# Optimization experiments

Hardware: AMD Instinct MI355X
Metric: run time of the kernel (lower is better)

Reference implementation:

```python
import jax, jax.numpy as jnp
import numpy as np

EPS = 1e-6          # AllReduceParams.eps for the fused RMSNorm
FP8_MAX = 448.0     # max finite magnitude of float8_e4m3fn


def setup_inputs() -> dict:
    key = jax.random.key(0)
    k1, k2, k3 = jax.random.split(key, 3)
    tp, T, H = 4, 4096, 8192  # tp ranks, tokens, hidden
    return {
        "input": jax.random.normal(k1, (tp, T, H), jnp.float32) * 0.05,
        "residual": jax.random.normal(k2, (T, H), jnp.float32),
        "norm_weight": jax.random.uniform(k3, (H,), jnp.float32, 0.5, 1.5),
        "scale": jnp.ones((1,), jnp.float32),  # static per-tensor FP8 scale
    }


def _fp8_e4m3_roundtrip(x):
    # Emulate e4m3 rounding; straight-through so the op stays differentiable.
    x = jnp.clip(x, -FP8_MAX, FP8_MAX)
    rounded = x.astype(jnp.float8_e4m3fn).astype(jnp.float32)
    return x + jax.lax.stop_gradient(rounded - x)


def reference(input, residual, norm_weight, scale):
    # All-reduce (sum over TP ranks) -- leading axis models the TP group.
    reduced = jnp.sum(input, axis=0)                 # [T, H]
    # Fused residual add.
    residual_out = reduced + residual                # [T, H]
    # Fused RMSNorm.
    var = jnp.mean(jnp.square(residual_out), axis=-1, keepdims=True)
    norm = residual_out * jax.lax.rsqrt(var + EPS) * norm_weight
    # Fused static per-tensor FP8 (e4m3) quantization: q = round_fp8(x * scale).
    quant = _fp8_e4m3_roundtrip(norm * scale)        # [T, H] fp8-rounded values
    return (quant, residual_out)
```

## Files before the change

### kernel.cpp

```cpp
#include <hip/hip_runtime.h>

constexpr int TP  = 4;
constexpr int TT  = 4096;
constexpr int HH  = 8192;
constexpr int BLK = 512;
constexpr int NJ  = HH / (BLK * 4);

typedef float f32x4 __attribute__((ext_vector_type(4)));

__device__ __forceinline__ unsigned swz(unsigned byte) {
    return byte ^ (((byte >> 9) & 7u) << 4);
}

__device__ __forceinline__ double fp8_rne_d(double x) {
    long long b = (long long)__double_as_longlong(fabs(x));
    int ee = (int)(b >> 52);
    if (ee < 1017) ee = 1017;
    long long se = (long long)(ee - 3);
    double step = __longlong_as_double(se << 52);
    double inv  = __longlong_as_double((2046 - se) << 52);
    return rint(x * inv) * step;
}

__global__ __launch_bounds__(BLK) void fused_ar_rms_fp8(
    const float* __restrict__ input,
    const float* __restrict__ residual,
    const float* __restrict__ weight,
    const float* __restrict__ scale,
    float* __restrict__ quant,
    float* __restrict__ resid_out)
{
    __shared__ float lds[HH];
    __shared__ float bcast;

    const int t   = blockIdx.x;
    const int tid = threadIdx.x;
    const size_t row   = (size_t)t * HH;
    const size_t plane = (size_t)TT * HH;

    const f32x4* i0 = (const f32x4*)(input + row);
    const f32x4* i1 = (const f32x4*)(input + plane + row);
    const f32x4* i2 = (const f32x4*)(input + 2 * plane + row);
    const f32x4* i3 = (const f32x4*)(input + 3 * plane + row);
    const f32x4* rr = (const f32x4*)(residual + row);
    f32x4* qo = (f32x4*)(quant + row);
    f32x4* ro = (f32x4*)(resid_out + row);
    const f32x4* wv = (const f32x4*)weight;

    float s[NJ * 4];

    #pragma unroll
    for (int j = 0; j < NJ; ++j) {
        const int idx = j * BLK + tid;
        f32x4 a = i0[idx];
        f32x4 b = i1[idx];
        f32x4 c = i2[idx];
        f32x4 d = i3[idx];
        f32x4 r = rr[idx];
        f32x4 sv;
        #pragma unroll
        for (int k = 0; k < 4; ++k) {
            float v = __fadd_rn(a[k], b[k]);
            v = __fadd_rn(v, c[k]);
            v = __fadd_rn(v, d[k]);
            v = __fadd_rn(v, r[k]);
            sv[k] = v;
            s[j * 4 + k] = v;
        }
        const unsigned byte = 16u * (unsigned)idx;
        *(f32x4*)((char*)lds + swz(byte)) = sv;
        ro[idx] = sv;
    }
    __syncthreads();

    if (tid < 64) {
        const unsigned base = 512u * (unsigned)tid;
        float r8[8];
        f32x4 q0 = *(const f32x4*)((const char*)lds + swz(base));
        f32x4 q1 = *(const f32x4*)((const char*)lds + swz(base + 16));
        #pragma unroll
        for (int k = 0; k < 4; ++k) {
            r8[k]     = __fmul_rn(q0[k], q0[k]);
            r8[4 + k] = __fmul_rn(q1[k], q1[k]);
        }
        #pragma unroll
        for (int i = 1; i < 16; ++i) {
            const unsigned b2 = base + 32u * i;
            q0 = *(const f32x4*)((const char*)lds + swz(b2));
            q1 = *(const f32x4*)((const char*)lds + swz(b2 + 16));
            #pragma unroll
            for (int k = 0; k < 4; ++k) {
                r8[k]     = __fadd_rn(r8[k],     __fmul_rn(q0[k], q0[k]));
                r8[4 + k] = __fadd_rn(r8[4 + k], __fmul_rn(q1[k], q1[k]));
            }
        }
        float res = __fadd_rn(
            __fadd_rn(__fadd_rn(r8[0], r8[1]), __fadd_rn(r8[2], r8[3])),
            __fadd_rn(__fadd_rn(r8[4], r8[5]), __fadd_rn(r8[6], r8[7])));
        #pragma unroll
        for (int m = 1; m < 64; m <<= 1)
            res = __fadd_rn(res, __shfl_xor(res, m, 64));

        const float mean = __fmul_rn(res, 1.0f / 8192.0f);
        const float v    = __fadd_rn(mean, 1e-6f);
        const float rinv = __fdiv_rn(1.0f, __fsqrt_rn(v));
        if (tid == 0) bcast = rinv;
    }
    __syncthreads();

    const float rinv = bcast;
    const float sc   = scale[0];

    #pragma unroll
    for (int j = 0; j < NJ; ++j) {
        const int idx = j * BLK + tid;
        f32x4 w4 = wv[idx];
        f32x4 qv;
        #pragma unroll
        for (int k = 0; k < 4; ++k) {
            float n = __fmul_rn(s[j * 4 + k], rinv);
            n = __fmul_rn(n, w4[k]);
            n = __fmul_rn(n, sc);
            n = fminf(fmaxf(n, -448.0f), 448.0f);
            qv[k] = (float)fp8_rne_d((double)n);
        }
        qo[idx] = qv;
    }
}

extern "C" void kernel_launch(void* const* d_in, const int* in_sizes, int n_in,
                              void* d_out, int out_size, void* d_ws, size_t ws_size,
                              hipStream_t stream) {
    const float* input    = (const float*)d_in[0];
    const float* residual = (const float*)d_in[1];
    const float* weight   = (const float*)d_in[2];
    const float* scale    = (const float*)d_in[3];
    float* quant     = (float*)d_out;
    float* resid_out = (float*)d_out + (size_t)TT * HH;

    fused_ar_rms_fp8<<<TT, BLK, 0, stream>>>(input, residual, weight, scale,
                                             quant, resid_out);
}
```

Measured before the change: 178.4 us.

## Process four rows per block with register prefetch of next row and nontemporal IO

Result: slower. 209.8 us (+17.6%).

```diff
diff --git a/kernel.cpp b/kernel.cpp
--- a/kernel.cpp
+++ b/kernel.cpp
@@ -5,11 +5,19 @@
 constexpr int HH  = 8192;
 constexpr int BLK = 512;
 constexpr int NJ  = HH / (BLK * 4);
+constexpr int RPB = 4;
+constexpr int GRID = TT / RPB;
 
 typedef float f32x4 __attribute__((ext_vector_type(4)));
 
 __device__ __forceinline__ unsigned swz(unsigned byte) {
     return byte ^ (((byte >> 9) & 7u) << 4);
+}
+
+__device__ __forceinline__ void barrier_lgkm() {
+    asm volatile("s_waitcnt lgkmcnt(0)" ::: "memory");
+    __builtin_amdgcn_s_barrier();
+    asm volatile("" ::: "memory");
 }
 
 __device__ __forceinline__ double fp8_rne_d(double x) {
@@ -22,7 +30,7 @@
     return rint(x * inv) * step;
 }
 
-__global__ __launch_bounds__(BLK) void fused_ar_rms_fp8(
+__global__ __launch_bounds__(BLK, 4) void fused_ar_rms_fp8(
     const float* __restrict__ input,
     const float* __restrict__ residual,
     const float* __restrict__ weight,
@@ -33,98 +41,127 @@
     __shared__ float lds[HH];
     __shared__ float bcast;
 
-    const int t   = blockIdx.x;
     const int tid = threadIdx.x;
-    const size_t row   = (size_t)t * HH;
     const size_t plane = (size_t)TT * HH;
+    const size_t row0  = (size_t)blockIdx.x * RPB * HH;
 
-    const f32x4* i0 = (const f32x4*)(input + row);
-    const f32x4* i1 = (const f32x4*)(input + plane + row);
-    const f32x4* i2 = (const f32x4*)(input + 2 * plane + row);
-    const f32x4* i3 = (const f32x4*)(input + 3 * plane + row);
-    const f32x4* rr = (const f32x4*)(residual + row);
-    f32x4* qo = (f32x4*)(quant + row);
-    f32x4* ro = (f32x4*)(resid_out + row);
     const f32x4* wv = (const f32x4*)weight;
+    const float sc = scale[0];
 
-    float s[NJ * 4];
+    f32x4 cur[5 * NJ];
 
-    #pragma unroll
-    for (int j = 0; j < NJ; ++j) {
-        const int idx = j * BLK + tid;
-        f32x4 a = i0[idx];
-        f32x4 b = i1[idx];
-        f32x4 c = i2[idx];
-        f32x4 d = i3[idx];
-        f32x4 r = rr[idx];
-        f32x4 sv;
+    {
+        const f32x4* i0 = (const f32x4*)(input + row0);
+        const f32x4* rr = (const f32x4*)(residual + row0);
         #pragma unroll
-        for (int k = 0; k < 4; ++k) {
-            float v = __fadd_rn(a[k], b[k]);
-            v = __fadd_rn(v, c[k]);
-            v = __fadd_rn(v, d[k]);
-            v = __fadd_rn(v, r[k]);
-            sv[k] = v;
-            s[j * 4 + k] = v;
+        for (int j = 0; j < NJ; ++j) {
+            const int idx = j * BLK + tid;
+            cur[j * 5 + 0] = __builtin_nontemporal_load(&i0[idx]);
+            cur[j * 5 + 1] = __builtin_nontemporal_load(&i0[plane / 4 + idx]);
+            cur[j * 5 + 2] = __builtin_nontemporal_load(&i0[2 * (plane / 4) + idx]);
+            cur[j * 5 + 3] = __builtin_nontemporal_load(&i0[3 * (plane / 4) + idx]);
+            cur[j * 5 + 4] = __builtin_nontemporal_load(&rr[idx]);
         }
-        const unsigned byte = 16u * (unsigned)idx;
-        *(f32x4*)((char*)lds + swz(byte)) = sv;
-        ro[idx] = sv;
     }
-    __syncthreads();
 
-    if (tid < 64) {
-        const unsigned base = 512u * (unsigned)tid;
-        float r8[8];
-        f32x4 q0 = *(const f32x4*)((const char*)lds + swz(base));
-        f32x4 q1 = *(const f32x4*)((const char*)lds + swz(base + 16));
+    for (int r = 0; r < RPB; ++r) {
+        const size_t row = row0 + (size_t)r * HH;
+        f32x4* qo = (f32x4*)(quant + row);
+        f32x4* ro = (f32x4*)(resid_out + row);
+
+        float s[NJ * 4];
+
         #pragma unroll
-        for (int k = 0; k < 4; ++k) {
-            r8[k]     = __fmul_rn(q0[k], q0[k]);
-            r8[4 + k] = __fmul_rn(q1[k], q1[k]);
-        }
-        #pragma unroll
-        for (int i = 1; i < 16; ++i) {
-            const unsigned b2 = base + 32u * i;
-            q0 = *(const f32x4*)((const char*)lds + swz(b2));
-            q1 = *(const f32x4*)((const char*)lds + swz(b2 + 16));
+        for (int j = 0; j < NJ; ++j) {
+            const int idx = j * BLK + tid;
+            f32x4 a = cur[j * 5 + 0], b = cur[j * 5 + 1];
+            f32x4 c = cur[j * 5 + 2], d = cur[j * 5 + 3];
+            f32x4 e = cur[j * 5 + 4];
+            f32x4 sv;
             #pragma unroll
             for (int k = 0; k < 4; ++k) {
-                r8[k]     = __fadd_rn(r8[k],     __fmul_rn(q0[k], q0[k]));
-                r8[4 + k] = __fadd_rn(r8[4 + k], __fmul_rn(q1[k], q1[k]));
+                float v = __fadd_rn(a[k], b[k]);
+                v = __fadd_rn(v, c[k]);
+                v = __fadd_rn(v, d[k]);
+                v = __fadd_rn(v, e[k]);
+                sv[k] = v;
+                s[j * 4 + k] = v;
+            }
+            *(f32x4*)((char*)lds + swz(16u * (unsigned)idx)) = sv;
+            __builtin_nontemporal_store(sv, &ro[idx]);
+        }
+
+        if (r + 1 < RPB) {
+            const size_t nrow = row + HH;
+            const f32x4* i0 = (const f32x4*)(input + nrow);
+            const f32x4* rr = (const f32x4*)(residual + nrow);
+            #pragma unroll
+            for (int j = 0; j < NJ; ++j) {
+                const int idx = j * BLK + tid;
+                cur[j * 5 + 0] = __builtin_nontemporal_load(&i0[idx]);
+                cur[j * 5 + 1] = __builtin_nontemporal_load(&i0[plane / 4 + idx]);
+                cur[j * 5 + 2] = __builtin_nontemporal_load(&i0[2 * (plane / 4) + idx]);
+                cur[j * 5 + 3] = __builtin_nontemporal_load(&i0[3 * (plane / 4) + idx]);
+                cur[j * 5 + 4] = __builtin_nontemporal_load(&rr[idx]);
             }
         }
-        float res = __fadd_rn(
-            __fadd_rn(__fadd_rn(r8[0], r8[1]), __fadd_rn(r8[2], r8[3])),
-            __fadd_rn(__fadd_rn(r8[4], r8[5]), __fadd_rn(r8[6], r8[7])));
+
+        barrier_lgkm();
+
+        if (tid < 64) {
+            const unsigned base = 512u * (unsigned)tid;
+            float r8[8];
+            f32x4 q0 = *(const f32x4*)((const char*)lds + swz(base));
+            f32x4 q1 = *(const f32x4*)((const char*)lds + swz(base + 16));
+            #pragma unroll
+            for (int k = 0; k < 4; ++k) {
+                r8[k]     = __fmul_rn(q0[k], q0[k]);
+                r8[4 + k] = __fmul_rn(q1[k], q1[k]);
+            }
+            #pragma unroll
+            for (int i = 1; i < 16; ++i) {
+                const unsigned b2 = base + 32u * i;
+                q0 = *(const f32x4*)((const char*)lds + swz(b2));
+                q1 = *(const f32x4*)((const char*)lds + swz(b2 + 16));
+                #pragma unroll
+                for (int k = 0; k < 4; ++k) {
+                    r8[k]     = __fadd_rn(r8[k],     __fmul_rn(q0[k], q0[k]));
+                    r8[4 + k] = __fadd_rn(r8[4 + k], __fmul_rn(q1[k], q1[k]));
+                }
+            }
+            float res = __fadd_rn(
+                __fadd_rn(__fadd_rn(r8[0], r8[1]), __fadd_rn(r8[2], r8[3])),
+                __fadd_rn(__fadd_rn(r8[4], r8[5]), __fadd_rn(r8[6], r8[7])));
+            #pragma unroll
+            for (int m = 1; m < 64; m <<= 1)
+                res = __fadd_rn(res, __shfl_xor(res, m, 64));
+
+            const float mean = __fmul_rn(res, 1.0f / 8192.0f);
+            const float v    = __fadd_rn(mean, 1e-6f);
+            const float rinv = __fdiv_rn(1.0f, __fsqrt_rn(v));
+            if (tid == 0) bcast = rinv;
+        }
+
+        barrier_lgkm();
+
+        const float rinv = bcast;
+
         #pragma unroll
-        for (int m = 1; m < 64; m <<= 1)
-            res = __fadd_rn(res, __shfl_xor(res, m, 64));
+        for (int j = 0; j < NJ; ++j) {
+            const int idx = j * BLK + tid;
+            f32x4 w4 = wv[idx];
+            f32x4 qv;
+            #pragma unroll
+            for (int k = 0; k < 4; ++k) {
+                float n = __fmul_rn(s[j * 4 + k], rinv);
+                n = __fmul_rn(n, w4[k]);
+                n = __fmul_rn(n, sc);
+                n = fminf(fmaxf(n, -448.0f), 448.0f);
+                qv[k] = (float)fp8_rne_d((double)n);
+            }
+            __builtin_nontemporal_store(qv, &qo[idx]);
+        }
 
-        const float mean = __fmul_rn(res, 1.0f / 8192.0f);
-        const float v    = __fadd_rn(mean, 1e-6f);
-        const float rinv = __fdiv_rn(1.0f, __fsqrt_rn(v));
-        if (tid == 0) bcast = rinv;
-    }
-    __syncthreads();
-
-    const float rinv = bcast;
-    const float sc   = scale[0];
-
-    #pragma unroll
-    for (int j = 0; j < NJ; ++j) {
-        const int idx = j * BLK + tid;
-        f32x4 w4 = wv[idx];
-        f32x4 qv;
-        #pragma unroll
-        for (int k = 0; k < 4; ++k) {
-            float n = __fmul_rn(s[j * 4 + k], rinv);
-            n = __fmul_rn(n, w4[k]);
-            n = __fmul_rn(n, sc);
-            n = fminf(fmaxf(n, -448.0f), 448.0f);
-            qv[k] = (float)fp8_rne_d((double)n);
-        }
-        qo[idx] = qv;
     }
 }
 
@@ -138,6 +175,6 @@
     float* quant     = (float*)d_out;
     float* resid_out = (float*)d_out + (size_t)TT * HH;
 
-    fused_ar_rms_fp8<<<TT, BLK, 0, stream>>>(input, residual, weight, scale,
-                                             quant, resid_out);
+    fused_ar_rms_fp8<<<GRID, BLK, 0, stream>>>(input, residual, weight, scale,
+                                               quant, resid_out);
 }
```
